# Kernel optimization log

Hardware: AMD Instinct MI355X
Metric: run time of the kernel (lower is better)

The kernel has to match this reference:

```python
import jax, jax.numpy as jnp
import numpy as np

N, E = 50000, 1600000
D_IN, H, N_REL, D_OUT = 518, 256, 10, 128


def setup_inputs() -> dict:
    key = jax.random.key(0)
    ks = jax.random.split(key, 20)
    def lin(k, fan_in, fan_out):
        bound = 1.0 / np.sqrt(fan_in)
        kw, kb = jax.random.split(k)
        W = jax.random.uniform(kw, (fan_in, fan_out), jnp.float32, -bound, bound)
        b = jax.random.uniform(kb, (fan_out,), jnp.float32, -bound, bound)
        return W, b
    x = jax.random.normal(ks[0], (N, D_IN), jnp.float32)
    edge_index = jax.random.randint(ks[1], (2, E), 0, N, jnp.int32)
    edge_attr = jax.random.randint(ks[2], (E,), 0, N_REL, jnp.int32)
    W_enc1, b_enc1 = lin(ks[3], D_IN, H)
    W_enc2, b_enc2 = lin(ks[4], H, H)
    emb_table = jax.random.normal(ks[5], (N_REL, H // 4), jnp.float32)
    W_g1, b_g1 = lin(ks[6], H, H)
    W_g2, b_g2 = lin(ks[7], H, H)
    W_g3, b_g3 = lin(ks[8], H, H)
    W_h1, b_h1 = lin(ks[9], H, H // 2)
    W_h2, b_h2 = lin(ks[10], H // 2, D_OUT)
    return dict(x=x, edge_index=edge_index, edge_attr=edge_attr,
                W_enc1=W_enc1, b_enc1=b_enc1, W_enc2=W_enc2, b_enc2=b_enc2,
                emb_table=emb_table,
                W_g1=W_g1, b_g1=b_g1, W_g2=W_g2, b_g2=b_g2, W_g3=W_g3, b_g3=b_g3,
                W_h1=W_h1, b_h1=b_h1, W_h2=W_h2, b_h2=b_h2)


def reference(x, edge_index, edge_attr,
              W_enc1, b_enc1, W_enc2, b_enc2, emb_table,
              W_g1, b_g1, W_g2, b_g2, W_g3, b_g3,
              W_h1, b_h1, W_h2, b_h2):
    src, dst = edge_index[0], edge_index[1]
    n = x.shape[0]
    # GCN symmetric normalization with self-loops: deg = 1 + in-degree
    deg = 1.0 + jax.ops.segment_sum(jnp.ones_like(src, jnp.float32), dst, num_segments=n)
    dis = deg ** -0.5                       # [N]
    norm_e = dis[src] * dis[dst]            # [E] edge norm
    self_norm = (dis * dis)[:, None]        # [N,1] self-loop norm

    def gcn(h, W, b):
        hw = h @ W                           # [N,H]
        agg = jax.ops.segment_sum(hw[src] * norm_e[:, None], dst, num_segments=n)
        return agg + hw * self_norm + b

    # node encoder (dropout is identity in eval)
    h = jax.nn.relu(x @ W_enc1 + b_enc1) @ W_enc2 + b_enc2
    _edge_emb = emb_table[edge_attr]         # computed as in original (unused downstream)
    h = jax.nn.relu(gcn(h, W_g1, b_g1))
    h = jax.nn.relu(gcn(h, W_g2, b_g2))
    h = jax.nn.relu(gcn(h, W_g3, b_g3))
    graph_repr = jnp.mean(h, axis=0, keepdims=True)   # batch=None path -> [1,H]
    out = jax.nn.relu(graph_repr @ W_h1 + b_h1) @ W_h2 + b_h2
    return out
```

## Files before the change

kernel.cpp:

```cpp
#include <hip/hip_runtime.h>

#define D_IN 518
#define HD 256
#define KP1 544

typedef __attribute__((ext_vector_type(8))) short bf16x8;
typedef __attribute__((ext_vector_type(4))) float f32x4;
typedef __attribute__((ext_vector_type(4), aligned(4))) float float4u;
typedef __attribute__((ext_vector_type(2))) unsigned int uint2v;
typedef __attribute__((ext_vector_type(4))) unsigned short ushort4v;

__device__ __forceinline__ float bf2f(unsigned short u) {
  union { unsigned int i; float f; } v; v.i = ((unsigned int)u) << 16; return v.f;
}
__device__ __forceinline__ unsigned short f2bf(float f) {
  union { float f; unsigned int i; } v; v.f = f;
  unsigned int r = (v.i + 0x7FFFu + ((v.i >> 16) & 1u)) >> 16;
  return (unsigned short)r;
}

__global__ void k_canary(float* __restrict__ out, float code) {
  out[threadIdx.x] = code;
}


__global__ void k_hist(const int* __restrict__ dst, int E, int* __restrict__ cnt) {
  int e = (blockIdx.x * blockDim.x + threadIdx.x) * 4;
  if (e < E) {
    int4 d = *(const int4*)(dst + e);
    atomicAdd(&cnt[d.x], 1);
    atomicAdd(&cnt[d.y], 1);
    atomicAdd(&cnt[d.z], 1);
    atomicAdd(&cnt[d.w], 1);
  }
}

__global__ void k_blocksum(const int* __restrict__ cnt, int n, int* __restrict__ bsum) {
  __shared__ int red[256];
  const int t = threadIdx.x;
  int v = blockIdx.x * 256 + t;
  red[t] = (v < n) ? cnt[v] : 0;
  __syncthreads();
  for (int d = 128; d > 0; d >>= 1) {
    if (t < d) red[t] += red[t + d];
    __syncthreads();
  }
  if (t == 0) bsum[blockIdx.x] = red[0];
}

__global__ void k_scan_mid(const int* __restrict__ bsum, int nb, int* __restrict__ bex) {
  __shared__ int s[256];
  const int t = threadIdx.x;
  int x = (t < nb) ? bsum[t] : 0;
  s[t] = x;
  __syncthreads();
  for (int d = 1; d < 256; d <<= 1) {
    int v = (t >= d) ? s[t - d] : 0;
    __syncthreads();
    s[t] += v;
    __syncthreads();
  }
  if (t < nb) bex[t] = s[t] - x;
}

__global__ void k_off(const int* __restrict__ cnt, int n, const int* __restrict__ bex,
                      int* __restrict__ off, int* __restrict__ cursor,
                      float* __restrict__ dis) {
  __shared__ int s[256];
  const int t = threadIdx.x;
  const int v = blockIdx.x * 256 + t;
  int c = (v < n) ? cnt[v] : 0;
  s[t] = c;
  __syncthreads();
  for (int d = 1; d < 256; d <<= 1) {
    int x = (t >= d) ? s[t - d] : 0;
    __syncthreads();
    s[t] += x;
    __syncthreads();
  }
  if (v < n) {
    int incl = bex[blockIdx.x] + s[t];
    off[v + 1] = incl;
    cursor[v] = incl - c;
    dis[v] = 1.0f / sqrtf(1.0f + (float)c);
    if (v == 0) off[0] = 0;
  }
}

__global__ void k_fill_range(const int* __restrict__ src, const int* __restrict__ dst, int E,
                             int* __restrict__ cursor, unsigned short* __restrict__ csr,
                             int lo, int hi) {
  int e = (blockIdx.x * blockDim.x + threadIdx.x) * 4;
  if (e < E) {
    int4 d = *(const int4*)(dst + e);
    int4 s = *(const int4*)(src + e);
    if (d.x >= lo && d.x < hi) csr[atomicAdd(&cursor[d.x], 1)] = (unsigned short)s.x;
    if (d.y >= lo && d.y < hi) csr[atomicAdd(&cursor[d.y], 1)] = (unsigned short)s.y;
    if (d.z >= lo && d.z < hi) csr[atomicAdd(&cursor[d.z], 1)] = (unsigned short)s.z;
    if (d.w >= lo && d.w < hi) csr[atomicAdd(&cursor[d.w], 1)] = (unsigned short)s.w;
  }
}


__global__ void k_wt(const float* __restrict__ W, int K, int N, int Kp,
                     unsigned short* __restrict__ Wt) {
  int idx = blockIdx.x * blockDim.x + threadIdx.x;
  if (idx < N * Kp) {
    int n = idx / Kp, k = idx - n * Kp;
    Wt[idx] = (k < K) ? f2bf(W[k * N + n]) : (unsigned short)0;
  }
}

__global__ void k_wt4(const float* __restrict__ a, const float* __restrict__ b,
                      const float* __restrict__ c, const float* __restrict__ d,
                      unsigned short* __restrict__ oa, unsigned short* __restrict__ ob,
                      unsigned short* __restrict__ oc, unsigned short* __restrict__ od) {
  const float* W = (blockIdx.y == 0) ? a : (blockIdx.y == 1) ? b : (blockIdx.y == 2) ? c : d;
  unsigned short* O = (blockIdx.y == 0) ? oa : (blockIdx.y == 1) ? ob : (blockIdx.y == 2) ? oc : od;
  int idx = blockIdx.x * blockDim.x + threadIdx.x;
  int n = idx >> 8, k = idx & 255;
  O[idx] = f2bf(W[k * HD + n]);
}


__global__ __launch_bounds__(256, 2)
void k_gemm_bt(const unsigned short* __restrict__ A, int lda, int M, int K,
               const unsigned short* __restrict__ Bt, int ldb,
               const float* __restrict__ bias, const float* __restrict__ rowscale,
               int do_relu,
               unsigned short* __restrict__ C, int ldc) {
  const int bid = blockIdx.x;
  const int pair = (bid >> 4) * 8 + (bid & 7);
  const int mtiles = (M + 127) >> 7;
  if (pair >= mtiles) return;
  const int m0 = pair << 7;
  const int n0 = ((bid >> 3) & 1) << 7;

  __shared__ unsigned short As[128 * 40];
  __shared__ unsigned short Bs[128 * 40];
  const int tid = threadIdx.x;
  const int lane = tid & 63, wave = tid >> 6;
  const int q = lane >> 4, l15 = lane & 15;
  const int wm = (wave & 1) * 64, wn = (wave >> 1) * 64;

  f32x4 acc[4][4];
#pragma unroll
  for (int i = 0; i < 4; i++)
#pragma unroll
    for (int j = 0; j < 4; j++) acc[i][j] = f32x4{0.f, 0.f, 0.f, 0.f};

  const int r0 = tid >> 2, kb = tid & 3;
  int gmA0 = m0 + r0;       if (gmA0 >= M) gmA0 = M - 1;
  int gmA1 = m0 + r0 + 64;  if (gmA1 >= M) gmA1 = M - 1;
  const unsigned short* Arow0 = A + (size_t)gmA0 * lda;
  const unsigned short* Arow1 = A + (size_t)gmA1 * lda;
  const unsigned short* Brow0 = Bt + (size_t)(n0 + r0) * ldb;
  const unsigned short* Brow1 = Bt + (size_t)(n0 + r0 + 64) * ldb;
  unsigned short* lA0 = &As[r0 * 40 + kb * 8];
  unsigned short* lA1 = &As[(r0 + 64) * 40 + kb * 8];
  unsigned short* lB0 = &Bs[r0 * 40 + kb * 8];
  unsigned short* lB1 = &Bs[(r0 + 64) * 40 + kb * 8];

  for (int k0 = 0; k0 < K; k0 += 32) {
    __syncthreads();
    const int gk = k0 + kb * 8;
    *(bf16x8*)lA0 = *(const bf16x8*)(Arow0 + gk);
    *(bf16x8*)lA1 = *(const bf16x8*)(Arow1 + gk);
    *(bf16x8*)lB0 = *(const bf16x8*)(Brow0 + gk);
    *(bf16x8*)lB1 = *(const bf16x8*)(Brow1 + gk);
    __syncthreads();

    bf16x8 af[4], bfr[4];
#pragma unroll
    for (int i = 0; i < 4; i++)
      af[i] = *(const bf16x8*)(&As[(wm + i * 16 + l15) * 40 + q * 8]);
#pragma unroll
    for (int j = 0; j < 4; j++)
      bfr[j] = *(const bf16x8*)(&Bs[(wn + j * 16 + l15) * 40 + q * 8]);
#pragma unroll
    for (int i = 0; i < 4; i++)
#pragma unroll
      for (int j = 0; j < 4; j++)
        acc[i][j] = __builtin_amdgcn_mfma_f32_16x16x32_bf16(af[i], bfr[j], acc[i][j], 0, 0, 0);
  }

#pragma unroll
  for (int j = 0; j < 4; j++) {
    const int col = n0 + wn + j * 16 + l15;
    const float bv = bias ? bias[col] : 0.f;
#pragma unroll
    for (int i = 0; i < 4; i++) {
#pragma unroll
      for (int rg = 0; rg < 4; rg++) {
        int gr = m0 + wm + i * 16 + q * 4 + rg;
        if (gr < M) {
          float v = acc[i][j][rg];
          if (rowscale) v *= rowscale[gr];
          v += bv;
          if (do_relu) v = fmaxf(v, 0.f);
          C[(size_t)gr * ldc + col] = f2bf(v);
        }
      }
    }
  }
}


__global__ __launch_bounds__(256, 2)
void k_gemm_f32in(const float* __restrict__ A, int lda, int M, int Kreal, int Kloop,
                  const unsigned short* __restrict__ Bt, int ldb,
                  const float* __restrict__ bias, int do_relu,
                  unsigned short* __restrict__ C, int ldc) {
  const int bid = blockIdx.x;
  const int pair = (bid >> 4) * 8 + (bid & 7);
  const int mtiles = (M + 127) >> 7;
  if (pair >= mtiles) return;
  const int m0 = pair << 7;
  const int n0 = ((bid >> 3) & 1) << 7;

  __shared__ unsigned short As[128 * 40];
  __shared__ unsigned short Bs[128 * 40];
  const int tid = threadIdx.x;
  const int lane = tid & 63, wave = tid >> 6;
  const int q = lane >> 4, l15 = lane & 15;
  const int wm = (wave & 1) * 64, wn = (wave >> 1) * 64;

  f32x4 acc[4][4];
#pragma unroll
  for (int i = 0; i < 4; i++)
#pragma unroll
    for (int j = 0; j < 4; j++) acc[i][j] = f32x4{0.f, 0.f, 0.f, 0.f};

  const int r0 = tid >> 2, kb = tid & 3;
  int gmA0 = m0 + r0;       if (gmA0 >= M) gmA0 = M - 1;
  int gmA1 = m0 + r0 + 64;  if (gmA1 >= M) gmA1 = M - 1;
  const float* Arow0 = A + (size_t)gmA0 * lda;
  const float* Arow1 = A + (size_t)gmA1 * lda;
  const unsigned short* Brow0 = Bt + (size_t)(n0 + r0) * ldb;
  const unsigned short* Brow1 = Bt + (size_t)(n0 + r0 + 64) * ldb;
  unsigned short* lA0 = &As[r0 * 40 + kb * 8];
  unsigned short* lA1 = &As[(r0 + 64) * 40 + kb * 8];
  unsigned short* lB0 = &Bs[r0 * 40 + kb * 8];
  unsigned short* lB1 = &Bs[(r0 + 64) * 40 + kb * 8];

  for (int k0 = 0; k0 < Kloop; k0 += 32) {
    __syncthreads();
    const int gk = k0 + kb * 8;
    if (gk + 8 <= Kreal) {
      float4u a0 = *(const float4u*)(Arow0 + gk);
      float4u a1 = *(const float4u*)(Arow0 + gk + 4);
      float4u b0 = *(const float4u*)(Arow1 + gk);
      float4u b1 = *(const float4u*)(Arow1 + gk + 4);
      bf16x8 t0, t1;
      t0[0] = (short)f2bf(a0.x); t0[1] = (short)f2bf(a0.y);
      t0[2] = (short)f2bf(a0.z); t0[3] = (short)f2bf(a0.w);
      t0[4] = (short)f2bf(a1.x); t0[5] = (short)f2bf(a1.y);
      t0[6] = (short)f2bf(a1.z); t0[7] = (short)f2bf(a1.w);
      t1[0] = (short)f2bf(b0.x); t1[1] = (short)f2bf(b0.y);
      t1[2] = (short)f2bf(b0.z); t1[3] = (short)f2bf(b0.w);
      t1[4] = (short)f2bf(b1.x); t1[5] = (short)f2bf(b1.y);
      t1[6] = (short)f2bf(b1.z); t1[7] = (short)f2bf(b1.w);
      *(bf16x8*)lA0 = t0;
      *(bf16x8*)lA1 = t1;
    } else {
      bf16x8 t0, t1;
#pragma unroll
      for (int t = 0; t < 8; t++) {
        int kk = gk + t;
        t0[t] = (short)((kk < Kreal) ? f2bf(Arow0[kk]) : (unsigned short)0);
        t1[t] = (short)((kk < Kreal) ? f2bf(Arow1[kk]) : (unsigned short)0);
      }
      *(bf16x8*)lA0 = t0;
      *(bf16x8*)lA1 = t1;
    }
    *(bf16x8*)lB0 = *(const bf16x8*)(Brow0 + gk);
    *(bf16x8*)lB1 = *(const bf16x8*)(Brow1 + gk);
    __syncthreads();

    bf16x8 af[4], bfr[4];
#pragma unroll
    for (int i = 0; i < 4; i++)
      af[i] = *(const bf16x8*)(&As[(wm + i * 16 + l15) * 40 + q * 8]);
#pragma unroll
    for (int j = 0; j < 4; j++)
      bfr[j] = *(const bf16x8*)(&Bs[(wn + j * 16 + l15) * 40 + q * 8]);
#pragma unroll
    for (int i = 0; i < 4; i++)
#pragma unroll
      for (int j = 0; j < 4; j++)
        acc[i][j] = __builtin_amdgcn_mfma_f32_16x16x32_bf16(af[i], bfr[j], acc[i][j], 0, 0, 0);
  }

#pragma unroll
  for (int j = 0; j < 4; j++) {
    const int col = n0 + wn + j * 16 + l15;
    const float bv = bias ? bias[col] : 0.f;
#pragma unroll
    for (int i = 0; i < 4; i++) {
#pragma unroll
      for (int rg = 0; rg < 4; rg++) {
        int gr = m0 + wm + i * 16 + q * 4 + rg;
        if (gr < M) {
          float v = acc[i][j][rg] + bv;
          if (do_relu) v = fmaxf(v, 0.f);
          C[(size_t)gr * ldc + col] = f2bf(v);
        }
      }
    }
  }
}


__global__ __launch_bounds__(256)
void k_agg(const unsigned short* __restrict__ hw,
           const int* __restrict__ off, const unsigned short* __restrict__ csr,
           const float* __restrict__ dis,
           const float* __restrict__ bias,
           unsigned short* __restrict__ hout, int n) {
  const int wave = threadIdx.x >> 6, lane = threadIdx.x & 63;
  const int v = blockIdx.x * 4 + wave;
  if (v >= n) return;
  const int cb = lane << 2;
  const unsigned short* hwcb = hw + cb;
  float a0 = 0.f, a1 = 0.f, a2 = 0.f, a3 = 0.f;

  const int e0 = off[v], e1 = off[v + 1];
  for (int e = e0; e < e1; e += 64) {
    int cnt = e1 - e; if (cnt > 64) cnt = 64;
    int sidx = 0;
    if (lane < cnt) sidx = (int)csr[e + lane];
    int j = 0;
    for (; j + 16 <= cnt; j += 16) {
      uint2v d[16];
#pragma unroll
      for (int p = 0; p < 16; ++p) {
        int sp = __builtin_amdgcn_readlane(sidx, j + p);
        d[p] = *(const uint2v*)(hwcb + ((size_t)sp << 8));
      }
#pragma unroll
      for (int p = 0; p < 16; ++p) {
        a0 += __uint_as_float(d[p][0] << 16);
        a1 += __uint_as_float(d[p][0] & 0xFFFF0000u);
        a2 += __uint_as_float(d[p][1] << 16);
        a3 += __uint_as_float(d[p][1] & 0xFFFF0000u);
      }
    }
    for (; j < cnt; j += 8) {
      uint2v d[8];
#pragma unroll
      for (int p = 0; p < 8; ++p) {
        if (j + p < cnt) {
          int sp = __builtin_amdgcn_readlane(sidx, j + p);
          d[p] = *(const uint2v*)(hwcb + ((size_t)sp << 8));
        }
      }
#pragma unroll
      for (int p = 0; p < 8; ++p) {
        if (j + p < cnt) {
          a0 += __uint_as_float(d[p][0] << 16);
          a1 += __uint_as_float(d[p][0] & 0xFFFF0000u);
          a2 += __uint_as_float(d[p][1] << 16);
          a3 += __uint_as_float(d[p][1] & 0xFFFF0000u);
        }
      }
    }
  }

  {
    uint2v ds_ = *(const uint2v*)(hwcb + ((size_t)v << 8));
    a0 += __uint_as_float(ds_[0] << 16);
    a1 += __uint_as_float(ds_[0] & 0xFFFF0000u);
    a2 += __uint_as_float(ds_[1] << 16);
    a3 += __uint_as_float(ds_[1] & 0xFFFF0000u);
  }
  const float dv = dis[v];
  const float4u bv = *(const float4u*)(bias + cb);
  ushort4v o;
  o[0] = f2bf(fmaxf(dv * a0 + bv.x, 0.f));
  o[1] = f2bf(fmaxf(dv * a1 + bv.y, 0.f));
  o[2] = f2bf(fmaxf(dv * a2 + bv.z, 0.f));
  o[3] = f2bf(fmaxf(dv * a3 + bv.w, 0.f));
  *(ushort4v*)(hout + ((size_t)v << 8) + cb) = o;
}


__global__ void k_colsum(const unsigned short* __restrict__ h, int n, float* __restrict__ gsum) {
  const int t = threadIdx.x;
  const int per = (n + gridDim.x - 1) / gridDim.x;
  const int rs = blockIdx.x * per;
  int re = rs + per; if (re > n) re = n;
  float s = 0.f;
  for (int r = rs; r < re; ++r) s += bf2f(h[(size_t)r * HD + t]);
  atomicAdd(&gsum[t], s);
}

__global__ void k_head(const float* __restrict__ gsum, float invN,
                       const float* __restrict__ Wh1, const float* __restrict__ bh1,
                       const float* __restrict__ Wh2, const float* __restrict__ bh2,
                       float* __restrict__ out) {
  __shared__ float g[256];
  __shared__ float t1[128];
  const int t = threadIdx.x;
  g[t] = gsum[t] * invN;
  g[t + 128] = gsum[t + 128] * invN;
  __syncthreads();
  float s = bh1[t];
  for (int k = 0; k < 256; ++k) s += g[k] * Wh1[k * 128 + t];
  t1[t] = fmaxf(s, 0.f);
  __syncthreads();
  float o = bh2[t];
  for (int j = 0; j < 128; ++j) o += t1[j] * Wh2[j * 128 + t];
  out[t] = o;
}


extern "C" void kernel_launch(void* const* d_in, const int* in_sizes, int n_in,
                              void* d_out, int out_size, void* d_ws, size_t ws_size,
                              hipStream_t stream) {
  float* outp = (float*)d_out;

  const float* x   = (const float*)d_in[0];
  const int* ei    = (const int*)d_in[1];
  const float* W1  = (const float*)d_in[3];
  const float* b1  = (const float*)d_in[4];
  const float* W2  = (const float*)d_in[5];
  const float* b2  = (const float*)d_in[6];
  const float* Wg1 = (const float*)d_in[8];
  const float* bg1 = (const float*)d_in[9];
  const float* Wg2 = (const float*)d_in[10];
  const float* bg2 = (const float*)d_in[11];
  const float* Wg3 = (const float*)d_in[12];
  const float* bg3 = (const float*)d_in[13];
  const float* Wh1 = (const float*)d_in[14];
  const float* bh1 = (const float*)d_in[15];
  const float* Wh2 = (const float*)d_in[16];
  const float* bh2 = (const float*)d_in[17];

  const int n = 50000;
  const int E = 1600000;
  const int nb = (n + 255) / 256;
  const int* srcp = ei;
  const int* dstp = ei + E;

  char* p = (char*)d_ws;
  size_t used = 0;
  auto alloc = [&](size_t bytes) -> char* {
    char* r = p; size_t rb = (bytes + 255) & ~((size_t)255);
    p += rb; used += rb; return r;
  };
  int*   cnt    = (int*)alloc((size_t)n * 4);
  int*   off    = (int*)alloc((size_t)(n + 1) * 4);
  int*   cursor = (int*)alloc((size_t)n * 4);
  float* dis    = (float*)alloc((size_t)n * 4);
  int*   bsum   = (int*)alloc((size_t)nb * 4);
  int*   bex    = (int*)alloc((size_t)nb * 4);
  float* gsum   = (float*)alloc(256 * 4);
  unsigned short* csr = (unsigned short*)alloc((size_t)E * 2);
  unsigned short* W1t  = (unsigned short*)alloc((size_t)HD * KP1 * 2);
  unsigned short* W2t  = (unsigned short*)alloc((size_t)HD * HD * 2);
  unsigned short* Wg1t = (unsigned short*)alloc((size_t)HD * HD * 2);
  unsigned short* Wg2t = (unsigned short*)alloc((size_t)HD * HD * 2);
  unsigned short* Wg3t = (unsigned short*)alloc((size_t)HD * HD * 2);
  unsigned short* P    = (unsigned short*)alloc((size_t)n * HD * 2);
  unsigned short* Q    = (unsigned short*)alloc((size_t)n * HD * 2);

  if (used > ws_size) { k_canary<<<1, 128, 0, stream>>>(outp, 90000.0f); return; }

  hipMemsetAsync(cnt, 0, (size_t)n * 4, stream);
  hipMemsetAsync(gsum, 0, 256 * 4, stream);

  k_hist<<<(E / 4 + 255) / 256, 256, 0, stream>>>(dstp, E, cnt);
  k_blocksum<<<nb, 256, 0, stream>>>(cnt, n, bsum);
  k_scan_mid<<<1, 256, 0, stream>>>(bsum, nb, bex);
  k_off<<<nb, 256, 0, stream>>>(cnt, n, bex, off, cursor, dis);
  {
    const int NPASS = 2, span = (n + NPASS - 1) / NPASS;
    for (int i = 0; i < NPASS; ++i) {
      int lo = i * span, hi = lo + span; if (hi > n) hi = n;
      k_fill_range<<<(E / 4 + 255) / 256, 256, 0, stream>>>(srcp, dstp, E, cursor, csr, lo, hi);
    }
  }

  k_wt<<<(HD * KP1 + 255) / 256, 256, 0, stream>>>(W1, D_IN, HD, KP1, W1t);
  {
    dim3 g4(HD * HD / 256, 4);
    k_wt4<<<g4, 256, 0, stream>>>(W2, Wg1, Wg2, Wg3, W2t, Wg1t, Wg2t, Wg3t);
  }

  const int mtiles = (n + 127) / 128;
  const int gblocks = ((mtiles + 7) / 8) * 16;
  const int ab = (n + 3) / 4;

  k_gemm_f32in<<<gblocks, 256, 0, stream>>>(x, D_IN, n, D_IN, KP1, W1t, KP1, b1, 1, P, HD);
  k_gemm_bt<<<gblocks, 256, 0, stream>>>(P, HD, n, HD, W2t, HD, b2, nullptr, 0, Q, HD);
  k_gemm_bt<<<gblocks, 256, 0, stream>>>(Q, HD, n, HD, Wg1t, HD, nullptr, dis, 0, P, HD);
  k_agg<<<ab, 256, 0, stream>>>(P, off, csr, dis, bg1, Q, n);
  k_gemm_bt<<<gblocks, 256, 0, stream>>>(Q, HD, n, HD, Wg2t, HD, nullptr, dis, 0, P, HD);
  k_agg<<<ab, 256, 0, stream>>>(P, off, csr, dis, bg2, Q, n);
  k_gemm_bt<<<gblocks, 256, 0, stream>>>(Q, HD, n, HD, Wg3t, HD, nullptr, dis, 0, P, HD);
  k_agg<<<ab, 256, 0, stream>>>(P, off, csr, dis, bg3, Q, n);

  k_colsum<<<256, 256, 0, stream>>>(Q, n, gsum);
  k_head<<<1, 128, 0, stream>>>(gsum, 1.0f / (float)n, Wh1, bh1, Wh2, bh2, outp);
}
```

Measured before the change: 889.0 us.

## Store GCN hidden features in column-sliced panels for cache-local aggregation

The GEMM epilogue can now write its output as eight 32-column panels, each holding all rows contiguously. The aggregation kernel is reworked so each block handles one panel for a chunk of 32 nodes. Each wave gathers neighbours with 8 edges by 8 column-lanes, then reduces across lanes with shuffles. Each panel (about 3.2 MB) is meant to stay cache-resident during the random gathers, instead of gathering across a 25 MB matrix. The cost is that the edge list is re-read once per slice, plus the shuffle reductions and writes strided by 32 columns in the GEMM.

```diff
diff --git a/kernel.cpp b/kernel.cpp
--- a/kernel.cpp
+++ b/kernel.cpp
@@ -128,7 +128,7 @@
                const unsigned short* __restrict__ Bt, int ldb,
                const float* __restrict__ bias, const float* __restrict__ rowscale,
                int do_relu,
-               unsigned short* __restrict__ C, int ldc) {
+               unsigned short* __restrict__ C, int ldc, int sliced, int Mp) {
   const int bid = blockIdx.x;
   const int pair = (bid >> 4) * 8 + (bid & 7);
   const int mtiles = (M + 127) >> 7;
@@ -184,10 +184,14 @@
         acc[i][j] = __builtin_amdgcn_mfma_f32_16x16x32_bf16(af[i], bfr[j], acc[i][j], 0, 0, 0);
   }
 
+  const size_t Mp32 = (size_t)Mp * 32;
 #pragma unroll
   for (int j = 0; j < 4; j++) {
     const int col = n0 + wn + j * 16 + l15;
     const float bv = bias ? bias[col] : 0.f;
+    unsigned short* cb = sliced ? (C + (size_t)(col >> 5) * Mp32 + (col & 31))
+                                : (C + col);
+    const int rstr = sliced ? 32 : ldc;
 #pragma unroll
     for (int i = 0; i < 4; i++) {
 #pragma unroll
@@ -198,7 +202,7 @@
           if (rowscale) v *= rowscale[gr];
           v += bv;
           if (do_relu) v = fmaxf(v, 0.f);
-          C[(size_t)gr * ldc + col] = f2bf(v);
+          cb[(size_t)gr * rstr] = f2bf(v);
         }
       }
     }
@@ -312,75 +316,78 @@
 
 
 __global__ __launch_bounds__(256)
-void k_agg(const unsigned short* __restrict__ hw,
-           const int* __restrict__ off, const unsigned short* __restrict__ csr,
-           const float* __restrict__ dis,
-           const float* __restrict__ bias,
-           unsigned short* __restrict__ hout, int n) {
+void k_agg_sl(const unsigned short* __restrict__ hw_sl, int Mp,
+              const int* __restrict__ off, const unsigned short* __restrict__ csr,
+              const float* __restrict__ dis, const float* __restrict__ bias,
+              unsigned short* __restrict__ hout, int n) {
+  const int slice = blockIdx.x & 7;
+  const int chunk = blockIdx.x >> 3;
   const int wave = threadIdx.x >> 6, lane = threadIdx.x & 63;
-  const int v = blockIdx.x * 4 + wave;
-  if (v >= n) return;
-  const int cb = lane << 2;
-  const unsigned short* hwcb = hw + cb;
-  float a0 = 0.f, a1 = 0.f, a2 = 0.f, a3 = 0.f;
-
-  const int e0 = off[v], e1 = off[v + 1];
-  for (int e = e0; e < e1; e += 64) {
-    int cnt = e1 - e; if (cnt > 64) cnt = 64;
-    int sidx = 0;
-    if (lane < cnt) sidx = (int)csr[e + lane];
-    int j = 0;
-    for (; j + 16 <= cnt; j += 16) {
-      uint2v d[16];
-#pragma unroll
-      for (int p = 0; p < 16; ++p) {
-        int sp = __builtin_amdgcn_readlane(sidx, j + p);
-        d[p] = *(const uint2v*)(hwcb + ((size_t)sp << 8));
+  const int eg = lane >> 3, cl = lane & 7;
+  const unsigned short* panel = hw_sl + (size_t)slice * ((size_t)Mp * 32) + (cl << 2);
+  const float4u bv = *(const float4u*)(bias + (slice << 5) + (cl << 2));
+  const int base = chunk << 5;
+
+  for (int v = base + wave; v < base + 32; v += 4) {
+    if (v >= n) break;
+    float a0 = 0.f, a1 = 0.f, a2 = 0.f, a3 = 0.f;
+    const int e0 = off[v], e1 = off[v + 1];
+    int e = e0;
+    for (; e + 32 <= e1; e += 32) {
+      uint2v d[4];
+#pragma unroll
+      for (int p = 0; p < 4; ++p) {
+        int sp = (int)csr[e + (p << 3) + eg];
+        d[p] = *(const uint2v*)(panel + ((size_t)sp << 5));
       }
 #pragma unroll
-      for (int p = 0; p < 16; ++p) {
+      for (int p = 0; p < 4; ++p) {
         a0 += __uint_as_float(d[p][0] << 16);
         a1 += __uint_as_float(d[p][0] & 0xFFFF0000u);
         a2 += __uint_as_float(d[p][1] << 16);
         a3 += __uint_as_float(d[p][1] & 0xFFFF0000u);
       }
     }
-    for (; j < cnt; j += 8) {
-      uint2v d[8];
-#pragma unroll
-      for (int p = 0; p < 8; ++p) {
-        if (j + p < cnt) {
-          int sp = __builtin_amdgcn_readlane(sidx, j + p);
-          d[p] = *(const uint2v*)(hwcb + ((size_t)sp << 8));
-        }
-      }
-#pragma unroll
-      for (int p = 0; p < 8; ++p) {
-        if (j + p < cnt) {
-          a0 += __uint_as_float(d[p][0] << 16);
-          a1 += __uint_as_float(d[p][0] & 0xFFFF0000u);
-          a2 += __uint_as_float(d[p][1] << 16);
-          a3 += __uint_as_float(d[p][1] & 0xFFFF0000u);
-        }
-      }
-    }
-  }
-
-  {
-    uint2v ds_ = *(const uint2v*)(hwcb + ((size_t)v << 8));
-    a0 += __uint_as_float(ds_[0] << 16);
-    a1 += __uint_as_float(ds_[0] & 0xFFFF0000u);
-    a2 += __uint_as_float(ds_[1] << 16);
-    a3 += __uint_as_float(ds_[1] & 0xFFFF0000u);
-  }
-  const float dv = dis[v];
-  const float4u bv = *(const float4u*)(bias + cb);
-  ushort4v o;
-  o[0] = f2bf(fmaxf(dv * a0 + bv.x, 0.f));
-  o[1] = f2bf(fmaxf(dv * a1 + bv.y, 0.f));
-  o[2] = f2bf(fmaxf(dv * a2 + bv.z, 0.f));
-  o[3] = f2bf(fmaxf(dv * a3 + bv.w, 0.f));
-  *(ushort4v*)(hout + ((size_t)v << 8) + cb) = o;
+    for (; e + 8 <= e1; e += 8) {
+      int sp = (int)csr[e + eg];
+      uint2v d = *(const uint2v*)(panel + ((size_t)sp << 5));
+      a0 += __uint_as_float(d[0] << 16);
+      a1 += __uint_as_float(d[0] & 0xFFFF0000u);
+      a2 += __uint_as_float(d[1] << 16);
+      a3 += __uint_as_float(d[1] & 0xFFFF0000u);
+    }
+    if (e < e1 && eg < (e1 - e)) {
+      int sp = (int)csr[e + eg];
+      uint2v d = *(const uint2v*)(panel + ((size_t)sp << 5));
+      a0 += __uint_as_float(d[0] << 16);
+      a1 += __uint_as_float(d[0] & 0xFFFF0000u);
+      a2 += __uint_as_float(d[1] << 16);
+      a3 += __uint_as_float(d[1] & 0xFFFF0000u);
+    }
+
+#pragma unroll
+    for (int m = 8; m <= 32; m <<= 1) {
+      a0 += __shfl_xor(a0, m, 64);
+      a1 += __shfl_xor(a1, m, 64);
+      a2 += __shfl_xor(a2, m, 64);
+      a3 += __shfl_xor(a3, m, 64);
+    }
+
+    if (eg == 0) {
+      uint2v ds_ = *(const uint2v*)(panel + ((size_t)v << 5));
+      a0 += __uint_as_float(ds_[0] << 16);
+      a1 += __uint_as_float(ds_[0] & 0xFFFF0000u);
+      a2 += __uint_as_float(ds_[1] << 16);
+      a3 += __uint_as_float(ds_[1] & 0xFFFF0000u);
+      const float dv = dis[v];
+      ushort4v o;
+      o[0] = f2bf(fmaxf(dv * a0 + bv.x, 0.f));
+      o[1] = f2bf(fmaxf(dv * a1 + bv.y, 0.f));
+      o[2] = f2bf(fmaxf(dv * a2 + bv.z, 0.f));
+      o[3] = f2bf(fmaxf(dv * a3 + bv.w, 0.f));
+      *(ushort4v*)(hout + ((size_t)v << 8) + (slice << 5) + (cl << 2)) = o;
+    }
+  }
 }
 
 
@@ -439,6 +446,7 @@
   const int n = 50000;
   const int E = 1600000;
   const int nb = (n + 255) / 256;
+  const int Mp = (n + 127) & ~127;
   const int* srcp = ei;
   const int* dstp = ei + E;
 
@@ -461,7 +469,7 @@
   unsigned short* Wg1t = (unsigned short*)alloc((size_t)HD * HD * 2);
   unsigned short* Wg2t = (unsigned short*)alloc((size_t)HD * HD * 2);
   unsigned short* Wg3t = (unsigned short*)alloc((size_t)HD * HD * 2);
-  unsigned short* P    = (unsigned short*)alloc((size_t)n * HD * 2);
+  unsigned short* P    = (unsigned short*)alloc((size_t)Mp * HD * 2);
   unsigned short* Q    = (unsigned short*)alloc((size_t)n * HD * 2);
 
   if (used > ws_size) { k_canary<<<1, 128, 0, stream>>>(outp, 90000.0f); return; }
@@ -489,16 +497,16 @@
 
   const int mtiles = (n + 127) / 128;
   const int gblocks = ((mtiles + 7) / 8) * 16;
-  const int ab = (n + 3) / 4;
+  const int agrid = ((n + 31) / 32) * 8;
 
   k_gemm_f32in<<<gblocks, 256, 0, stream>>>(x, D_IN, n, D_IN, KP1, W1t, KP1, b1, 1, P, HD);
-  k_gemm_bt<<<gblocks, 256, 0, stream>>>(P, HD, n, HD, W2t, HD, b2, nullptr, 0, Q, HD);
-  k_gemm_bt<<<gblocks, 256, 0, stream>>>(Q, HD, n, HD, Wg1t, HD, nullptr, dis, 0, P, HD);
-  k_agg<<<ab, 256, 0, stream>>>(P, off, csr, dis, bg1, Q, n);
-  k_gemm_bt<<<gblocks, 256, 0, stream>>>(Q, HD, n, HD, Wg2t, HD, nullptr, dis, 0, P, HD);
-  k_agg<<<ab, 256, 0, stream>>>(P, off, csr, dis, bg2, Q, n);
-  k_gemm_bt<<<gblocks, 256, 0, stream>>>(Q, HD, n, HD, Wg3t, HD, nullptr, dis, 0, P, HD);
-  k_agg<<<ab, 256, 0, stream>>>(P, off, csr, dis, bg3, Q, n);
+  k_gemm_bt<<<gblocks, 256, 0, stream>>>(P, HD, n, HD, W2t, HD, b2, nullptr, 0, Q, HD, 0, Mp);
+  k_gemm_bt<<<gblocks, 256, 0, stream>>>(Q, HD, n, HD, Wg1t, HD, nullptr, dis, 0, P, HD, 1, Mp);
+  k_agg_sl<<<agrid, 256, 0, stream>>>(P, Mp, off, csr, dis, bg1, Q, n);
+  k_gemm_bt<<<gblocks, 256, 0, stream>>>(Q, HD, n, HD, Wg2t, HD, nullptr, dis, 0, P, HD, 1, Mp);
+  k_agg_sl<<<agrid, 256, 0, stream>>>(P, Mp, off, csr, dis, bg2, Q, n);
+  k_gemm_bt<<<gblocks, 256, 0, stream>>>(Q, HD, n, HD, Wg3t, HD, nullptr, dis, 0, P, HD, 1, Mp);
+  k_agg_sl<<<agrid, 256, 0, stream>>>(P, Mp, off, csr, dis, bg3, Q, n);
 
   k_colsum<<<256, 256, 0, stream>>>(Q, n, gsum);
   k_head<<<1, 128, 0, stream>>>(gsum, 1.0f / (float)n, Wh1, bh1, Wh2, bh2, outp);
```

Result: slower. 1.002 ms (+12.7%).
